# Kernel optimization log

Measured on AMD Instinct MI355X. Metric: run time of the kernel, lower is better.

The kernel has to match this reference:

```python
import jax, jax.numpy as jnp
import numpy as np

NEG = -1000000.0  # mask fill value used by original sequence_mask

def setup_inputs() -> dict:
    key = jax.random.key(0)
    k1, k2, k3, k4 = jax.random.split(key, 4)
    B, S, D = 32, 2048, 64
    queries = jax.random.normal(k1, (B, S, D), dtype=jnp.float32)
    keys = jax.random.normal(k2, (B, S, D), dtype=jnp.float32)
    values = jax.random.normal(k3, (B, S, D), dtype=jnp.float32)
    valid_lens = jax.random.randint(k4, (B,), 1, S + 1, dtype=jnp.int64)
    return {"queries": queries, "keys": keys, "values": values, "valid_lens": valid_lens}

def reference(queries, keys, values, valid_lens):
    d = queries.shape[-1]
    # [B, Sq, Sk]
    scores = jnp.einsum('bqd,bkd->bqk', queries, keys) / jnp.sqrt(jnp.asarray(d, queries.dtype))
    # valid_lens is 1D: one length per batch row, broadcast over all query rows
    kv_idx = jnp.arange(scores.shape[-1])  # [Sk]
    mask = kv_idx[None, None, :] < valid_lens[:, None, None]  # [B,1,Sk] broadcast
    scores = jnp.where(mask, scores, jnp.asarray(NEG, scores.dtype))
    weights = jax.nn.softmax(scores, axis=-1)
    # dropout p=0.0 -> identity
    return jnp.einsum('bqk,bkd->bqd', weights, values)
```

## Files before the change

### kernel.cpp

```cpp
#include <hip/hip_runtime.h>
#include <hip/hip_bf16.h>

typedef __attribute__((ext_vector_type(8))) short bf16x8;
typedef __attribute__((ext_vector_type(4))) float f32x4;
typedef __attribute__((ext_vector_type(16))) float f32x16;
typedef __attribute__((ext_vector_type(4))) unsigned int u32x4;

#define BATCH 32
#define SEQ   2048
#define PSTR  20
#define KSTR  72
#define VSTR  36
#define LOG2E 1.44269504088896340736f
#define QSCALE (0.125f * LOG2E)
#define NEGL  (-1000000.0f * LOG2E)

__device__ __forceinline__ unsigned int pk2(float lo, float hi) {
    __hip_bfloat162 h2 = __float22bfloat162_rn(make_float2(lo, hi));
    return *reinterpret_cast<unsigned int*>(&h2);
}

__device__ __forceinline__ void plswap(unsigned int& a, unsigned int& b) {
    asm volatile("v_permlane32_swap_b32 %0, %1" : "+v"(a), "+v"(b));
}

__global__ void prep_vl(const int* __restrict__ VL, int* __restrict__ meta) {
    __shared__ int sv[BATCH];
    const int t = threadIdx.x;
    int odd = (t < 16) ? VL[2 * t + 1] : 0;
    const bool is64 = (__ballot(odd != 0) == 0ULL);
    if (t < BATCH) {
        int x = is64 ? VL[2 * t] : VL[t];
        x = x < 0 ? 0 : (x > SEQ ? SEQ : x);
        sv[t] = x;
    }
    __syncthreads();
    if (t < BATCH) {
        const int x = sv[t];
        int rank = 0;
        for (int j = 0; j < BATCH; ++j) {
            const int y = sv[j];
            rank += (y > x) || (y == x && j < t);
        }
        meta[rank] = x;
        meta[BATCH + rank] = t;
    }
}

__global__ __launch_bounds__(256) void prepkv(const float* __restrict__ Kp,
                                              const float* __restrict__ Vp,
                                              const int* __restrict__ VL,
                                              short* __restrict__ Kw,
                                              short* __restrict__ Vw,
                                              int* __restrict__ meta) {
    __shared__ unsigned int l[64 * VSTR];
    __shared__ int sv[BATCH];
    __shared__ int svl;
    const int tid = threadIdx.x;
    if (blockIdx.x == BATCH * 32) {
        if (tid < 64) {
            int odd = (tid < 16) ? VL[2 * tid + 1] : 0;
            const bool is64 = (__ballot(odd != 0) == 0ULL);
            if (tid < BATCH) {
                int x = is64 ? VL[2 * tid] : VL[tid];
                x = x < 0 ? 0 : (x > SEQ ? SEQ : x);
                sv[tid] = x;
            }
            asm volatile("s_waitcnt lgkmcnt(0)" ::: "memory");
            if (tid < BATCH) {
                const int x = sv[tid];
                int rank = 0;
                for (int j = 0; j < BATCH; ++j) {
                    const int y = sv[j];
                    rank += (y > x) || (y == x && j < tid);
                }
                meta[rank] = x;
                meta[BATCH + rank] = tid;
            }
        }
        return;
    }
    const int b = blockIdx.x >> 5, kt = blockIdx.x & 31, kb = kt * 64;
    if (tid < 64) {
        int odd = (tid < 16) ? VL[2 * tid + 1] : 0;
        const bool is64 = (__ballot(odd != 0) == 0ULL);
        if (tid == 0) {
            int x = is64 ? VL[2 * b] : VL[b];
            x = x < 0 ? 0 : (x > SEQ ? SEQ : x);
            svl = x;
        }
    }
    __syncthreads();
    if (kb >= ((svl + 63) & ~63)) return;
    const float* Kv = Kp + ((size_t)b * SEQ + kb) * 64;
    const float* Vb = Vp + ((size_t)b * SEQ + kb) * 64;
    const size_t tbase = (size_t)(b * 32 + kt) * 8192;

    #pragma unroll
    for (int h = 0; h < 2; ++h) {
        const int c = tid + h * 256;
        const int kh = c >> 8, kf = (c >> 6) & 3, ln = c & 63;
        const int key = kh * 32 + (ln & 31), col = kf * 16 + (ln >> 5) * 8;
        f32x4 a = *(const f32x4*)(Kv + key * 64 + col);
        f32x4 d = *(const f32x4*)(Kv + key * 64 + col + 4);
        u32x4 w;
        w.x = pk2(a[0], a[1]); w.y = pk2(a[2], a[3]);
        w.z = pk2(d[0], d[1]); w.w = pk2(d[2], d[3]);
        *(u32x4*)((char*)Kw + tbase + (size_t)c * 16) = w;
    }
    #pragma unroll
    for (int h = 0; h < 2; ++h) {
        const int u = tid + h * 256;
        const int d4 = (u & 3) + ((u >> 7) << 2);
        const int kp = (u >> 2) & 31;
        f32x4 a = *(const f32x4*)(Vb + (2 * kp) * 64 + d4 * 4);
        f32x4 c = *(const f32x4*)(Vb + (2 * kp + 1) * 64 + d4 * 4);
        #pragma unroll
        for (int j = 0; j < 4; ++j)
            l[(d4 * 4 + j) * VSTR + kp] = pk2(a[j], c[j]);
    }
    __syncthreads();
    #pragma unroll
    for (int h = 0; h < 2; ++h) {
        const int cV = tid + h * 256;
        const int kh = cV >> 8, q = (cV >> 6) & 3, ln = cV & 63;
        const int d = (q >> 1) * 32 + (ln & 31);
        const int cc = kh * 4 + (q & 1) * 2 + (ln >> 5);
        u32x4 w = *(const u32x4*)&l[d * VSTR + 4 * cc];
        *(u32x4*)((char*)Vw + tbase + (size_t)cV * 16) = w;
    }
}

__global__ __launch_bounds__(512, 4)
void attn_fwd(const float* __restrict__ Qp, const short* __restrict__ Kw,
              const short* __restrict__ Vw, const int* __restrict__ meta,
              float* __restrict__ Out) {
    constexpr int S = SEQ;
    __shared__ float mA[2 * 2048];
    __shared__ float mB[2 * 2048];
    __shared__ float lA[128], lB[128];

    const int tid  = threadIdx.x;
    const int wave = tid >> 6, lane = tid & 63;
    const int r31 = lane & 31, hi = lane >> 5;
    const int qh = wave >> 2, kh = wave & 3;

    const int x  = blockIdx.x & 7;
    const int i  = blockIdx.x >> 3;
    const int ss = i >> 5;
    const int qt = i & 31;
    const int slot = (ss == 0) ? x : (ss == 1) ? 15 - x : (ss == 2) ? 16 + x : 31 - x;

    const int vl = meta[slot], batch = meta[BATCH + slot];
    const int nG = (vl + 31) >> 5;
    const int ntw = (nG > kh) ? ((nG - kh + 3) >> 2) : 0;

    const char* kw = (const char*)Kw + ((size_t)batch * 64 + kh) * 4096 + lane * 16;
    const char* vw = (const char*)Vw + ((size_t)batch * 64 + kh) * 4096 + lane * 16;

    bf16x8 qf[4];
    {
        const float* qb = Qp + ((size_t)batch * S + qt * 64 + qh * 32 + r31) * 64 + hi * 8;
        #pragma unroll
        for (int kf = 0; kf < 4; ++kf) {
            f32x4 a = *(const f32x4*)(qb + kf * 16);
            f32x4 c = *(const f32x4*)(qb + kf * 16 + 4);
            union { bf16x8 v; unsigned int u[4]; } qq;
            qq.u[0] = pk2(a[0] * QSCALE, a[1] * QSCALE);
            qq.u[1] = pk2(a[2] * QSCALE, a[3] * QSCALE);
            qq.u[2] = pk2(c[0] * QSCALE, c[1] * QSCALE);
            qq.u[3] = pk2(c[2] * QSCALE, c[3] * QSCALE);
            qf[kf] = qq.v;
        }
    }

    f32x16 o0, o1, zv;
    #pragma unroll
    for (int r = 0; r < 16; ++r) { o0[r] = 0.f; o1[r] = 0.f; zv[r] = 0.f; }
    float lpart = 0.f;

    bf16x8 kk0, kk1, kk2, kk3, vv0, vv1, vv2, vv3;
    if (ntw > 0) {
        kk0 = *(const bf16x8*)(kw);
        kk1 = *(const bf16x8*)(kw + 1024);
        kk2 = *(const bf16x8*)(kw + 2048);
        kk3 = *(const bf16x8*)(kw + 3072);
        vv0 = *(const bf16x8*)(vw);
        vv1 = *(const bf16x8*)(vw + 1024);
        vv2 = *(const bf16x8*)(vw + 2048);
        vv3 = *(const bf16x8*)(vw + 3072);
    }

    for (int t = 0; t < ntw; ++t) {
        f32x16 st;
        __builtin_amdgcn_s_setprio(1);
        st = __builtin_amdgcn_mfma_f32_32x32x16_bf16(kk0, qf[0], zv, 0, 0, 0);
        st = __builtin_amdgcn_mfma_f32_32x32x16_bf16(kk1, qf[1], st, 0, 0, 0);
        st = __builtin_amdgcn_mfma_f32_32x32x16_bf16(kk2, qf[2], st, 0, 0, 0);
        st = __builtin_amdgcn_mfma_f32_32x32x16_bf16(kk3, qf[3], st, 0, 0, 0);
        __builtin_amdgcn_s_setprio(0);

        if (t + 1 < ntw) {
            const char* p = kw + (size_t)(t + 1) * 16384;
            kk0 = *(const bf16x8*)(p);
            kk1 = *(const bf16x8*)(p + 1024);
            kk2 = *(const bf16x8*)(p + 2048);
            kk3 = *(const bf16x8*)(p + 3072);
        }

        const int rem = vl - (kh + 4 * t) * 32;
        if (rem < 32) {
            #pragma unroll
            for (int r = 0; r < 16; ++r) {
                const int kl = 4 * hi + (r & 3) + 8 * (r >> 2);
                st[r] = (kl < rem) ? st[r] : NEGL;
            }
        }

        #pragma unroll
        for (int r = 0; r < 16; ++r) st[r] = __builtin_amdgcn_exp2f(st[r]);
        {
            const float a0 = (st[0] + st[1]) + (st[2] + st[3]);
            const float a1 = (st[4] + st[5]) + (st[6] + st[7]);
            const float a2 = (st[8] + st[9]) + (st[10] + st[11]);
            const float a3 = (st[12] + st[13]) + (st[14] + st[15]);
            lpart += (a0 + a1) + (a2 + a3);
        }

        union { bf16x8 v; unsigned int u[4]; } pf0, pf1;
        {
            unsigned int x0 = pk2(st[0], st[1]),   y0 = pk2(st[4], st[5]);
            unsigned int x1 = pk2(st[2], st[3]),   y1 = pk2(st[6], st[7]);
            plswap(x0, y0); plswap(x1, y1);
            pf0.u[0] = x0; pf0.u[1] = x1; pf0.u[2] = y0; pf0.u[3] = y1;
            unsigned int x2 = pk2(st[8], st[9]),   y2 = pk2(st[12], st[13]);
            unsigned int x3 = pk2(st[10], st[11]), y3 = pk2(st[14], st[15]);
            plswap(x2, y2); plswap(x3, y3);
            pf1.u[0] = x2; pf1.u[1] = x3; pf1.u[2] = y2; pf1.u[3] = y3;
        }

        __builtin_amdgcn_s_setprio(1);
        o0 = __builtin_amdgcn_mfma_f32_32x32x16_bf16(vv0, pf0.v, o0, 0, 0, 0);
        o0 = __builtin_amdgcn_mfma_f32_32x32x16_bf16(vv1, pf1.v, o0, 0, 0, 0);
        o1 = __builtin_amdgcn_mfma_f32_32x32x16_bf16(vv2, pf0.v, o1, 0, 0, 0);
        o1 = __builtin_amdgcn_mfma_f32_32x32x16_bf16(vv3, pf1.v, o1, 0, 0, 0);
        __builtin_amdgcn_s_setprio(0);

        if (t + 1 < ntw) {
            const char* p = vw + (size_t)(t + 1) * 16384;
            vv0 = *(const bf16x8*)(p);
            vv1 = *(const bf16x8*)(p + 1024);
            vv2 = *(const bf16x8*)(p + 2048);
            vv3 = *(const bf16x8*)(p + 3072);
        }
    }

    float lw = lpart + __shfl_xor(lpart, 32);

    if (kh == 1 || kh == 3) {
        float* m = (kh == 1) ? mA : mB;
        float* lv = (kh == 1) ? lA : lB;
        #pragma unroll
        for (int r = 0; r < 16; ++r) m[qh * 2048 + r * 64 + lane] = o0[r];
        #pragma unroll
        for (int r = 0; r < 16; ++r) m[qh * 2048 + (16 + r) * 64 + lane] = o1[r];
        lv[qh * 64 + lane] = lw;
    }
    __syncthreads();
    if (kh == 0 || kh == 2) {
        const float* m = (kh == 0) ? mA : mB;
        const float* lv = (kh == 0) ? lA : lB;
        #pragma unroll
        for (int r = 0; r < 16; ++r) o0[r] += m[qh * 2048 + r * 64 + lane];
        #pragma unroll
        for (int r = 0; r < 16; ++r) o1[r] += m[qh * 2048 + (16 + r) * 64 + lane];
        lw += lv[qh * 64 + lane];
    }
    __syncthreads();
    if (kh == 2) {
        #pragma unroll
        for (int r = 0; r < 16; ++r) mA[qh * 2048 + r * 64 + lane] = o0[r];
        #pragma unroll
        for (int r = 0; r < 16; ++r) mA[qh * 2048 + (16 + r) * 64 + lane] = o1[r];
        lA[qh * 64 + lane] = lw;
    }
    __syncthreads();
    if (kh == 0) {
        #pragma unroll
        for (int r = 0; r < 16; ++r) o0[r] += mA[qh * 2048 + r * 64 + lane];
        #pragma unroll
        for (int r = 0; r < 16; ++r) o1[r] += mA[qh * 2048 + (16 + r) * 64 + lane];
        lw += lA[qh * 64 + lane];
        const float inv = (lw > 0.f) ? 1.0f / lw : 0.f;
        const size_t orow = ((size_t)batch * S + qt * 64 + qh * 32 + r31) * 64;
        #pragma unroll
        for (int g4 = 0; g4 < 4; ++g4) {
            f32x4 w;
            #pragma unroll
            for (int j = 0; j < 4; ++j) w[j] = o0[g4 * 4 + j] * inv;
            *(f32x4*)(Out + orow + g4 * 8 + hi * 4) = w;
        }
        #pragma unroll
        for (int g4 = 0; g4 < 4; ++g4) {
            f32x4 w;
            #pragma unroll
            for (int j = 0; j < 4; ++j) w[j] = o1[g4 * 4 + j] * inv;
            *(f32x4*)(Out + orow + 32 + g4 * 8 + hi * 4) = w;
        }
    }
}

__device__ __forceinline__ void load_tile_fb(const float* __restrict__ Kb,
                                             const float* __restrict__ Vb,
                                             int tid, f32x4 kv[4], f32x4 vv[4]) {
    #pragma unroll
    for (int h = 0; h < 4; ++h) {
        const int c = tid + h * 256;
        kv[h] = *(const f32x4*)(Kb + (c >> 4) * 64 + (c & 15) * 4);
    }
    #pragma unroll
    for (int h = 0; h < 2; ++h) {
        const int u  = tid + h * 256;
        const int d4 = (u & 3) + ((u >> 7) << 2);
        const int kp = (u >> 2) & 31;
        vv[2 * h]     = *(const f32x4*)(Vb + (2 * kp) * 64 + d4 * 4);
        vv[2 * h + 1] = *(const f32x4*)(Vb + (2 * kp + 1) * 64 + d4 * 4);
    }
}

__global__ __launch_bounds__(256, 4)
void attn_fb(const float* __restrict__ Qp, const float* __restrict__ Kp,
             const float* __restrict__ Vp, const int* __restrict__ meta,
             float* __restrict__ Out) {
    constexpr int S = SEQ;
    constexpr int qtiles = S >> 6;
    __shared__ short        lK [64 * KSTR];
    __shared__ unsigned int lVt[64 * VSTR];
    __shared__ unsigned int lPt[4 * 32 * PSTR];
    const int tid = threadIdx.x;
    const int wave = tid >> 6, lane = tid & 63;
    const int l15 = lane & 15, grp = lane >> 4;
    const int slot = blockIdx.x / qtiles, qt = blockIdx.x % qtiles;
    const int vl = meta[slot], batch = meta[BATCH + slot];
    const int ntiles = (vl + 63) >> 6;
    const float* Kb = Kp + (size_t)batch * S * 64;
    const float* Vb = Vp + (size_t)batch * S * 64;
    bf16x8 qf[2];
    {
        const float* qb = Qp + ((size_t)batch * S + qt * 64 + wave * 16 + l15) * 64 + grp * 8;
        #pragma unroll
        for (int kf = 0; kf < 2; ++kf) {
            f32x4 a = *(const f32x4*)(qb + kf * 32);
            f32x4 b = *(const f32x4*)(qb + kf * 32 + 4);
            union { bf16x8 v; unsigned int u[4]; } qq;
            qq.u[0] = pk2(a[0], a[1]); qq.u[1] = pk2(a[2], a[3]);
            qq.u[2] = pk2(b[0], b[1]); qq.u[3] = pk2(b[2], b[3]);
            qf[kf] = qq.v;
        }
    }
    f32x4 o[4] = {{0.f,0.f,0.f,0.f},{0.f,0.f,0.f,0.f},{0.f,0.f,0.f,0.f},{0.f,0.f,0.f,0.f}};
    float mrun = -INFINITY, lrun = 0.f;
    unsigned int* pw = &lPt[wave * 32 * PSTR];
    f32x4 kv[4], vv[4];
    if (ntiles > 0) load_tile_fb(Kb, Vb, tid, kv, vv);
    for (int kt = 0; kt < ntiles; ++kt) {
        const int kb = kt * 64;
        __syncthreads();
        #pragma unroll
        for (int h = 0; h < 4; ++h) {
            const int c = tid + h * 256;
            const int row = c >> 4, col = (c & 15) * 4;
            union { f32x4 f; float e[4]; } x; x.f = kv[h];
            unsigned int* dst = (unsigned int*)&lK[row * KSTR + col];
            dst[0] = pk2(x.e[0], x.e[1]); dst[1] = pk2(x.e[2], x.e[3]);
        }
        #pragma unroll
        for (int h = 0; h < 2; ++h) {
            const int u  = tid + h * 256;
            const int d4 = (u & 3) + ((u >> 7) << 2);
            const int kp = (u >> 2) & 31;
            union { f32x4 f; float e[4]; } a, b;
            a.f = vv[2 * h]; b.f = vv[2 * h + 1];
            #pragma unroll
            for (int j = 0; j < 4; ++j)
                lVt[(d4 * 4 + j) * VSTR + kp] = pk2(a.e[j], b.e[j]);
        }
        if (kt + 1 < ntiles) load_tile_fb(Kb + (size_t)(kb + 64) * 64, Vb + (size_t)(kb + 64) * 64, tid, kv, vv);
        __syncthreads();
        f32x4 st[4] = {{0.f,0.f,0.f,0.f},{0.f,0.f,0.f,0.f},{0.f,0.f,0.f,0.f},{0.f,0.f,0.f,0.f}};
        #pragma unroll
        for (int kf = 0; kf < 2; ++kf) {
            #pragma unroll
            for (int ct = 0; ct < 4; ++ct) {
                bf16x8 kfr = *(const bf16x8*)&lK[(ct * 16 + l15) * KSTR + kf * 32 + grp * 8];
                st[ct] = __builtin_amdgcn_mfma_f32_16x16x32_bf16(kfr, qf[kf], st[ct], 0, 0, 0);
            }
        }
        #pragma unroll
        for (int ct = 0; ct < 4; ++ct)
            #pragma unroll
            for (int r = 0; r < 4; ++r) {
                const bool valid = (kb + ct * 16 + grp * 4 + r) < vl;
                st[ct][r] = valid ? st[ct][r] * (0.125f * LOG2E) : NEGL;
            }
        float t0 = fmaxf(fmaxf(st[0][0], st[0][1]), fmaxf(st[0][2], st[0][3]));
        float t1 = fmaxf(fmaxf(st[1][0], st[1][1]), fmaxf(st[1][2], st[1][3]));
        float t2 = fmaxf(fmaxf(st[2][0], st[2][1]), fmaxf(st[2][2], st[2][3]));
        float t3 = fmaxf(fmaxf(st[3][0], st[3][1]), fmaxf(st[3][2], st[3][3]));
        float tm = fmaxf(fmaxf(t0, t1), fmaxf(t2, t3));
        tm = fmaxf(tm, __shfl_xor(tm, 16));
        tm = fmaxf(tm, __shfl_xor(tm, 32));
        const float mnew  = fmaxf(mrun, tm);
        const float alpha = exp2f(mrun - mnew);
        mrun = mnew;
        lrun *= alpha;
        #pragma unroll
        for (int dt = 0; dt < 4; ++dt)
            #pragma unroll
            for (int r = 0; r < 4; ++r) o[dt][r] *= alpha;
        float rs = 0.f;
        #pragma unroll
        for (int ct = 0; ct < 4; ++ct) {
            #pragma unroll
            for (int r = 0; r < 4; ++r) {
                st[ct][r] = exp2f(st[ct][r] - mrun);
                rs += st[ct][r];
            }
            #pragma unroll
            for (int a = 0; a < 2; ++a)
                pw[(ct * 8 + grp * 2 + a) * PSTR + l15] = pk2(st[ct][2 * a], st[ct][2 * a + 1]);
        }
        rs += __shfl_xor(rs, 16);
        rs += __shfl_xor(rs, 32);
        lrun += rs;
        asm volatile("s_waitcnt lgkmcnt(0)" ::: "memory");
        #pragma unroll
        for (int kk = 0; kk < 2; ++kk) {
            union { bf16x8 v; unsigned int u[4]; } pf;
            #pragma unroll
            for (int jj = 0; jj < 4; ++jj)
                pf.u[jj] = pw[(kk * 16 + grp * 4 + jj) * PSTR + l15];
            #pragma unroll
            for (int dt = 0; dt < 4; ++dt) {
                bf16x8 vf = *(const bf16x8*)&lVt[(dt * 16 + l15) * VSTR + kk * 16 + grp * 4];
                o[dt] = __builtin_amdgcn_mfma_f32_16x16x32_bf16(vf, pf.v, o[dt], 0, 0, 0);
            }
        }
    }
    const float inv = (lrun > 0.f) ? 1.0f / lrun : 0.f;
    const size_t orow = ((size_t)batch * S + qt * 64 + wave * 16 + l15) * 64;
    #pragma unroll
    for (int dt = 0; dt < 4; ++dt) {
        f32x4 w = o[dt];
        w[0] *= inv; w[1] *= inv; w[2] *= inv; w[3] *= inv;
        *(f32x4*)(Out + orow + dt * 16 + grp * 4) = w;
    }
}

extern "C" void kernel_launch(void* const* d_in, const int* in_sizes, int n_in,
                              void* d_out, int out_size, void* d_ws, size_t ws_size,
                              hipStream_t stream) {
    const float* Q  = (const float*)d_in[0];
    const float* K  = (const float*)d_in[1];
    const float* V  = (const float*)d_in[2];
    const int*   VL = (const int*)d_in[3];
    int* meta = (int*)d_ws;
    const size_t need = 512 + 2 * (size_t)BATCH * SEQ * 64 * sizeof(short);
    if (ws_size >= need) {
        short* Kw = (short*)((char*)d_ws + 512);
        short* Vw = Kw + (size_t)BATCH * SEQ * 64;
        prepkv<<<dim3(BATCH * 32 + 1), dim3(256), 0, stream>>>(K, V, VL, Kw, Vw, meta);
        attn_fwd<<<dim3(BATCH * 32), dim3(512), 0, stream>>>(Q, Kw, Vw, meta, (float*)d_out);
    } else {
        prep_vl<<<1, 64, 0, stream>>>(VL, meta);
        attn_fb<<<dim3(BATCH * (SEQ >> 6)), dim3(256), 0, stream>>>(Q, K, V, meta, (float*)d_out);
    }
}
```

Baseline: 126.1 us.

## Have each wave process both 32-row query halves to reuse K/V fragments

```diff
diff --git a/kernel.cpp b/kernel.cpp
--- a/kernel.cpp
+++ b/kernel.cpp
@@ -131,19 +131,19 @@
     }
 }
 
-__global__ __launch_bounds__(512, 4)
+__global__ __launch_bounds__(256, 2)
 void attn_fwd(const float* __restrict__ Qp, const short* __restrict__ Kw,
               const short* __restrict__ Vw, const int* __restrict__ meta,
               float* __restrict__ Out) {
     constexpr int S = SEQ;
-    __shared__ float mA[2 * 2048];
-    __shared__ float mB[2 * 2048];
+    __shared__ float mA[4 * 1024];
+    __shared__ float mB[4 * 1024];
     __shared__ float lA[128], lB[128];
 
     const int tid  = threadIdx.x;
-    const int wave = tid >> 6, lane = tid & 63;
+    const int kh   = tid >> 6;
+    const int lane = tid & 63;
     const int r31 = lane & 31, hi = lane >> 5;
-    const int qh = wave >> 2, kh = wave & 3;
 
     const int x  = blockIdx.x & 7;
     const int i  = blockIdx.x >> 3;
@@ -158,26 +158,36 @@
     const char* kw = (const char*)Kw + ((size_t)batch * 64 + kh) * 4096 + lane * 16;
     const char* vw = (const char*)Vw + ((size_t)batch * 64 + kh) * 4096 + lane * 16;
 
-    bf16x8 qf[4];
+    bf16x8 qfA[4], qfB[4];
     {
-        const float* qb = Qp + ((size_t)batch * S + qt * 64 + qh * 32 + r31) * 64 + hi * 8;
+        const float* qa = Qp + ((size_t)batch * S + qt * 64 + r31) * 64 + hi * 8;
+        const float* qb = qa + 32 * 64;
         #pragma unroll
         for (int kf = 0; kf < 4; ++kf) {
-            f32x4 a = *(const f32x4*)(qb + kf * 16);
-            f32x4 c = *(const f32x4*)(qb + kf * 16 + 4);
+            f32x4 a = *(const f32x4*)(qa + kf * 16);
+            f32x4 c = *(const f32x4*)(qa + kf * 16 + 4);
             union { bf16x8 v; unsigned int u[4]; } qq;
             qq.u[0] = pk2(a[0] * QSCALE, a[1] * QSCALE);
             qq.u[1] = pk2(a[2] * QSCALE, a[3] * QSCALE);
             qq.u[2] = pk2(c[0] * QSCALE, c[1] * QSCALE);
             qq.u[3] = pk2(c[2] * QSCALE, c[3] * QSCALE);
-            qf[kf] = qq.v;
-        }
-    }
-
-    f32x16 o0, o1, zv;
-    #pragma unroll
-    for (int r = 0; r < 16; ++r) { o0[r] = 0.f; o1[r] = 0.f; zv[r] = 0.f; }
-    float lpart = 0.f;
+            qfA[kf] = qq.v;
+            f32x4 e = *(const f32x4*)(qb + kf * 16);
+            f32x4 f = *(const f32x4*)(qb + kf * 16 + 4);
+            qq.u[0] = pk2(e[0] * QSCALE, e[1] * QSCALE);
+            qq.u[1] = pk2(e[2] * QSCALE, e[3] * QSCALE);
+            qq.u[2] = pk2(f[0] * QSCALE, f[1] * QSCALE);
+            qq.u[3] = pk2(f[2] * QSCALE, f[3] * QSCALE);
+            qfB[kf] = qq.v;
+        }
+    }
+
+    f32x16 oA0, oA1, oB0, oB1, zv;
+    #pragma unroll
+    for (int r = 0; r < 16; ++r) {
+        oA0[r] = 0.f; oA1[r] = 0.f; oB0[r] = 0.f; oB1[r] = 0.f; zv[r] = 0.f;
+    }
+    float lpA = 0.f, lpB = 0.f;
 
     bf16x8 kk0, kk1, kk2, kk3, vv0, vv1, vv2, vv3;
     if (ntw > 0) {
@@ -192,12 +202,16 @@
     }
 
     for (int t = 0; t < ntw; ++t) {
-        f32x16 st;
+        f32x16 sA, sB;
         __builtin_amdgcn_s_setprio(1);
-        st = __builtin_amdgcn_mfma_f32_32x32x16_bf16(kk0, qf[0], zv, 0, 0, 0);
-        st = __builtin_amdgcn_mfma_f32_32x32x16_bf16(kk1, qf[1], st, 0, 0, 0);
-        st = __builtin_amdgcn_mfma_f32_32x32x16_bf16(kk2, qf[2], st, 0, 0, 0);
-        st = __builtin_amdgcn_mfma_f32_32x32x16_bf16(kk3, qf[3], st, 0, 0, 0);
+        sA = __builtin_amdgcn_mfma_f32_32x32x16_bf16(kk0, qfA[0], zv, 0, 0, 0);
+        sB = __builtin_amdgcn_mfma_f32_32x32x16_bf16(kk0, qfB[0], zv, 0, 0, 0);
+        sA = __builtin_amdgcn_mfma_f32_32x32x16_bf16(kk1, qfA[1], sA, 0, 0, 0);
+        sB = __builtin_amdgcn_mfma_f32_32x32x16_bf16(kk1, qfB[1], sB, 0, 0, 0);
+        sA = __builtin_amdgcn_mfma_f32_32x32x16_bf16(kk2, qfA[2], sA, 0, 0, 0);
+        sB = __builtin_amdgcn_mfma_f32_32x32x16_bf16(kk2, qfB[2], sB, 0, 0, 0);
+        sA = __builtin_amdgcn_mfma_f32_32x32x16_bf16(kk3, qfA[3], sA, 0, 0, 0);
+        sB = __builtin_amdgcn_mfma_f32_32x32x16_bf16(kk3, qfB[3], sB, 0, 0, 0);
         __builtin_amdgcn_s_setprio(0);
 
         if (t + 1 < ntw) {
@@ -213,37 +227,59 @@
             #pragma unroll
             for (int r = 0; r < 16; ++r) {
                 const int kl = 4 * hi + (r & 3) + 8 * (r >> 2);
-                st[r] = (kl < rem) ? st[r] : NEGL;
-            }
-        }
-
-        #pragma unroll
-        for (int r = 0; r < 16; ++r) st[r] = __builtin_amdgcn_exp2f(st[r]);
+                const bool v = (kl < rem);
+                sA[r] = v ? sA[r] : NEGL;
+                sB[r] = v ? sB[r] : NEGL;
+            }
+        }
+
+        #pragma unroll
+        for (int r = 0; r < 16; ++r) {
+            sA[r] = __builtin_amdgcn_exp2f(sA[r]);
+            sB[r] = __builtin_amdgcn_exp2f(sB[r]);
+        }
         {
-            const float a0 = (st[0] + st[1]) + (st[2] + st[3]);
-            const float a1 = (st[4] + st[5]) + (st[6] + st[7]);
-            const float a2 = (st[8] + st[9]) + (st[10] + st[11]);
-            const float a3 = (st[12] + st[13]) + (st[14] + st[15]);
-            lpart += (a0 + a1) + (a2 + a3);
-        }
-
-        union { bf16x8 v; unsigned int u[4]; } pf0, pf1;
+            const float a0 = (sA[0] + sA[1]) + (sA[2] + sA[3]);
+            const float a1 = (sA[4] + sA[5]) + (sA[6] + sA[7]);
+            const float a2 = (sA[8] + sA[9]) + (sA[10] + sA[11]);
+            const float a3 = (sA[12] + sA[13]) + (sA[14] + sA[15]);
+            lpA += (a0 + a1) + (a2 + a3);
+            const float b0 = (sB[0] + sB[1]) + (sB[2] + sB[3]);
+            const float b1 = (sB[4] + sB[5]) + (sB[6] + sB[7]);
+            const float b2 = (sB[8] + sB[9]) + (sB[10] + sB[11]);
+            const float b3 = (sB[12] + sB[13]) + (sB[14] + sB[15]);
+            lpB += (b0 + b1) + (b2 + b3);
+        }
+
+        union { bf16x8 v; unsigned int u[4]; } pA0, pA1, pB0, pB1;
         {
-            unsigned int x0 = pk2(st[0], st[1]),   y0 = pk2(st[4], st[5]);
-            unsigned int x1 = pk2(st[2], st[3]),   y1 = pk2(st[6], st[7]);
+            unsigned int x0 = pk2(sA[0], sA[1]),   y0 = pk2(sA[4], sA[5]);
+            unsigned int x1 = pk2(sA[2], sA[3]),   y1 = pk2(sA[6], sA[7]);
             plswap(x0, y0); plswap(x1, y1);
-            pf0.u[0] = x0; pf0.u[1] = x1; pf0.u[2] = y0; pf0.u[3] = y1;
-            unsigned int x2 = pk2(st[8], st[9]),   y2 = pk2(st[12], st[13]);
-            unsigned int x3 = pk2(st[10], st[11]), y3 = pk2(st[14], st[15]);
+            pA0.u[0] = x0; pA0.u[1] = x1; pA0.u[2] = y0; pA0.u[3] = y1;
+            unsigned int x2 = pk2(sA[8], sA[9]),   y2 = pk2(sA[12], sA[13]);
+            unsigned int x3 = pk2(sA[10], sA[11]), y3 = pk2(sA[14], sA[15]);
             plswap(x2, y2); plswap(x3, y3);
-            pf1.u[0] = x2; pf1.u[1] = x3; pf1.u[2] = y2; pf1.u[3] = y3;
+            pA1.u[0] = x2; pA1.u[1] = x3; pA1.u[2] = y2; pA1.u[3] = y3;
+            unsigned int z0 = pk2(sB[0], sB[1]),   w0 = pk2(sB[4], sB[5]);
+            unsigned int z1 = pk2(sB[2], sB[3]),   w1 = pk2(sB[6], sB[7]);
+            plswap(z0, w0); plswap(z1, w1);
+            pB0.u[0] = z0; pB0.u[1] = z1; pB0.u[2] = w0; pB0.u[3] = w1;
+            unsigned int z2 = pk2(sB[8], sB[9]),   w2 = pk2(sB[12], sB[13]);
+            unsigned int z3 = pk2(sB[10], sB[11]), w3 = pk2(sB[14], sB[15]);
+            plswap(z2, w2); plswap(z3, w3);
+            pB1.u[0] = z2; pB1.u[1] = z3; pB1.u[2] = w2; pB1.u[3] = w3;
         }
 
         __builtin_amdgcn_s_setprio(1);
-        o0 = __builtin_amdgcn_mfma_f32_32x32x16_bf16(vv0, pf0.v, o0, 0, 0, 0);
-        o0 = __builtin_amdgcn_mfma_f32_32x32x16_bf16(vv1, pf1.v, o0, 0, 0, 0);
-        o1 = __builtin_amdgcn_mfma_f32_32x32x16_bf16(vv2, pf0.v, o1, 0, 0, 0);
-        o1 = __builtin_amdgcn_mfma_f32_32x32x16_bf16(vv3, pf1.v, o1, 0, 0, 0);
+        oA0 = __builtin_amdgcn_mfma_f32_32x32x16_bf16(vv0, pA0.v, oA0, 0, 0, 0);
+        oB0 = __builtin_amdgcn_mfma_f32_32x32x16_bf16(vv0, pB0.v, oB0, 0, 0, 0);
+        oA0 = __builtin_amdgcn_mfma_f32_32x32x16_bf16(vv1, pA1.v, oA0, 0, 0, 0);
+        oB0 = __builtin_amdgcn_mfma_f32_32x32x16_bf16(vv1, pB1.v, oB0, 0, 0, 0);
+        oA1 = __builtin_amdgcn_mfma_f32_32x32x16_bf16(vv2, pA0.v, oA1, 0, 0, 0);
+        oB1 = __builtin_amdgcn_mfma_f32_32x32x16_bf16(vv2, pB0.v, oB1, 0, 0, 0);
+        oA1 = __builtin_amdgcn_mfma_f32_32x32x16_bf16(vv3, pA1.v, oA1, 0, 0, 0);
+        oB1 = __builtin_amdgcn_mfma_f32_32x32x16_bf16(vv3, pB1.v, oB1, 0, 0, 0);
         __builtin_amdgcn_s_setprio(0);
 
         if (t + 1 < ntw) {
@@ -255,57 +291,74 @@
         }
     }
 
-    float lw = lpart + __shfl_xor(lpart, 32);
+    float lwA = lpA + __shfl_xor(lpA, 32);
+    float lwB = lpB + __shfl_xor(lpB, 32);
 
     if (kh == 1 || kh == 3) {
-        float* m = (kh == 1) ? mA : mB;
+        float* m  = (kh == 1) ? mA : mB;
         float* lv = (kh == 1) ? lA : lB;
         #pragma unroll
-        for (int r = 0; r < 16; ++r) m[qh * 2048 + r * 64 + lane] = o0[r];
-        #pragma unroll
-        for (int r = 0; r < 16; ++r) m[qh * 2048 + (16 + r) * 64 + lane] = o1[r];
-        lv[qh * 64 + lane] = lw;
+        for (int r = 0; r < 16; ++r) {
+            m[0 * 1024 + r * 64 + lane] = oA0[r];
+            m[1 * 1024 + r * 64 + lane] = oA1[r];
+            m[2 * 1024 + r * 64 + lane] = oB0[r];
+            m[3 * 1024 + r * 64 + lane] = oB1[r];
+        }
+        lv[lane] = lwA; lv[64 + lane] = lwB;
     }
     __syncthreads();
     if (kh == 0 || kh == 2) {
-        const float* m = (kh == 0) ? mA : mB;
+        const float* m  = (kh == 0) ? mA : mB;
         const float* lv = (kh == 0) ? lA : lB;
         #pragma unroll
-        for (int r = 0; r < 16; ++r) o0[r] += m[qh * 2048 + r * 64 + lane];
-        #pragma unroll
-        for (int r = 0; r < 16; ++r) o1[r] += m[qh * 2048 + (16 + r) * 64 + lane];
-        lw += lv[qh * 64 + lane];
+        for (int r = 0; r < 16; ++r) {
+            oA0[r] += m[0 * 1024 + r * 64 + lane];
+            oA1[r] += m[1 * 1024 + r * 64 + lane];
+            oB0[r] += m[2 * 1024 + r * 64 + lane];
+            oB1[r] += m[3 * 1024 + r * 64 + lane];
+        }
+        lwA += lv[lane]; lwB += lv[64 + lane];
     }
     __syncthreads();
     if (kh == 2) {
         #pragma unroll
-        for (int r = 0; r < 16; ++r) mA[qh * 2048 + r * 64 + lane] = o0[r];
-        #pragma unroll
-        for (int r = 0; r < 16; ++r) mA[qh * 2048 + (16 + r) * 64 + lane] = o1[r];
-        lA[qh * 64 + lane] = lw;
+        for (int r = 0; r < 16; ++r) {
+            mA[0 * 1024 + r * 64 + lane] = oA0[r];
+            mA[1 * 1024 + r * 64 + lane] = oA1[r];
+            mA[2 * 1024 + r * 64 + lane] = oB0[r];
+            mA[3 * 1024 + r * 64 + lane] = oB1[r];
+        }
+        lA[lane] = lwA; lA[64 + lane] = lwB;
     }
     __syncthreads();
     if (kh == 0) {
         #pragma unroll
-        for (int r = 0; r < 16; ++r) o0[r] += mA[qh * 2048 + r * 64 + lane];
-        #pragma unroll
-        for (int r = 0; r < 16; ++r) o1[r] += mA[qh * 2048 + (16 + r) * 64 + lane];
-        lw += lA[qh * 64 + lane];
-        const float inv = (lw > 0.f) ? 1.0f / lw : 0.f;
-        const size_t orow = ((size_t)batch * S + qt * 64 + qh * 32 + r31) * 64;
+        for (int r = 0; r < 16; ++r) {
+            oA0[r] += mA[0 * 1024 + r * 64 + lane];
+            oA1[r] += mA[1 * 1024 + r * 64 + lane];
+            oB0[r] += mA[2 * 1024 + r * 64 + lane];
+            oB1[r] += mA[3 * 1024 + r * 64 + lane];
+        }
+        lwA += lA[lane]; lwB += lA[64 + lane];
+        const float invA = (lwA > 0.f) ? 1.0f / lwA : 0.f;
+        const float invB = (lwB > 0.f) ? 1.0f / lwB : 0.f;
+        const size_t orowA = ((size_t)batch * S + qt * 64 + r31) * 64;
+        const size_t orowB = orowA + (size_t)32 * 64;
         #pragma unroll
         for (int g4 = 0; g4 < 4; ++g4) {
             f32x4 w;
             #pragma unroll
-            for (int j = 0; j < 4; ++j) w[j] = o0[g4 * 4 + j] * inv;
-            *(f32x4*)(Out + orow + g4 * 8 + hi * 4) = w;
-        }
-        #pragma unroll
-        for (int g4 = 0; g4 < 4; ++g4) {
-            f32x4 w;
-            #pragma unroll
-            for (int j = 0; j < 4; ++j) w[j] = o1[g4 * 4 + j] * inv;
-            *(f32x4*)(Out + orow + 32 + g4 * 8 + hi * 4) = w;
+            for (int j = 0; j < 4; ++j) w[j] = oA0[g4 * 4 + j] * invA;
+            *(f32x4*)(Out + orowA + g4 * 8 + hi * 4) = w;
+            #pragma unroll
+            for (int j = 0; j < 4; ++j) w[j] = oA1[g4 * 4 + j] * invA;
+            *(f32x4*)(Out + orowA + 32 + g4 * 8 + hi * 4) = w;
+            #pragma unroll
+            for (int j = 0; j < 4; ++j) w[j] = oB0[g4 * 4 + j] * invB;
+            *(f32x4*)(Out + orowB + g4 * 8 + hi * 4) = w;
+            #pragma unroll
+            for (int j = 0; j < 4; ++j) w[j] = oB1[g4 * 4 + j] * invB;
+            *(f32x4*)(Out + orowB + 32 + g4 * 8 + hi * 4) = w;
         }
     }
 }
@@ -470,7 +523,7 @@
         short* Kw = (short*)((char*)d_ws + 512);
         short* Vw = Kw + (size_t)BATCH * SEQ * 64;
         prepkv<<<dim3(BATCH * 32 + 1), dim3(256), 0, stream>>>(K, V, VL, Kw, Vw, meta);
-        attn_fwd<<<dim3(BATCH * 32), dim3(512), 0, stream>>>(Q, Kw, Vw, meta, (float*)d_out);
+        attn_fwd<<<dim3(BATCH * 32), dim3(256), 0, stream>>>(Q, Kw, Vw, meta, (float*)d_out);
     } else {
         prep_vl<<<1, 64, 0, stream>>>(VL, meta);
         attn_fb<<<dim3(BATCH * (SEQ >> 6)), dim3(256), 0, stream>>>(Q, K, V, meta, (float*)d_out);
```

After: 119.3 us. 1.06x faster.
